# Kernel tuning notes

Hardware: AMD Instinct MI355X
Metric: run time of the kernel (lower is better)

Reference implementation:

```python
import jax, jax.numpy as jnp
import numpy as np

NUM_HEADS = 16
HIDDEN = 1024
HEAD_DIM = HIDDEN // NUM_HEADS
B, L = 1, 2048


def setup_inputs() -> dict:
    key = jax.random.key(0)
    ks = jax.random.split(key, 5)
    scale = 1.0 / np.sqrt(HIDDEN)
    x = jax.random.normal(ks[0], (B, L, HIDDEN), dtype=jnp.float32)
    Wq = jax.random.normal(ks[1], (HIDDEN, HIDDEN), dtype=jnp.float32) * scale
    Wk = jax.random.normal(ks[2], (HIDDEN, HIDDEN), dtype=jnp.float32) * scale
    Wv = jax.random.normal(ks[3], (HIDDEN, HIDDEN), dtype=jnp.float32) * scale
    Wo = jax.random.normal(ks[4], (HIDDEN, HIDDEN), dtype=jnp.float32) * scale
    return {"x": x, "Wq": Wq, "Wk": Wk, "Wv": Wv, "Wo": Wo}


def reference(x, Wq, Wk, Wv, Wo):
    Bx, Lx, _ = x.shape
    # nn.Linear computes x @ W.T (bias=False)
    q = (x @ Wq.T).reshape(Bx, Lx, NUM_HEADS, HEAD_DIM)
    k = (x @ Wk.T).reshape(Bx, Lx, NUM_HEADS, HEAD_DIM)
    v = (x @ Wv.T).reshape(Bx, Lx, NUM_HEADS, HEAD_DIM)
    # elu(.)+1 feature map
    q = jax.nn.elu(q) + 1.0
    k = jax.nn.elu(k) + 1.0
    # causal linear-attention state via cumsum of kv outer products
    kv = jnp.einsum('blhd,blhe->blhde', k, v)           # [B,L,H,D,D]
    kv_cumsum = jnp.cumsum(kv, axis=1)
    k_cumsum = jnp.cumsum(k, axis=1)
    out = jnp.einsum('blhd,blhde->blhe', q, kv_cumsum)   # [B,L,H,D]
    denom = jnp.clip(jnp.einsum('blhd,blhd->blh', q, k_cumsum), 1e-6, None)
    out = out / denom[..., None]
    return out.reshape(Bx, Lx, HIDDEN) @ Wo.T
```

## Files before the change

kernel.cpp:

```cpp
#include <hip/hip_runtime.h>
#include <hip/hip_bf16.h>

typedef __attribute__((ext_vector_type(8))) short short8;
typedef __attribute__((ext_vector_type(4))) float floatx4;
typedef __attribute__((ext_vector_type(8))) unsigned short ushortx8;
typedef __attribute__((ext_vector_type(4))) unsigned short ushortx4;
typedef unsigned short u16;

#define HIDDEN 1024
#define NH 16
#define HD 64
#define SEQ 2048
#define CHUNK 128
#define NCHUNK (SEQ / CHUNK)

__device__ __forceinline__ u16 f2bf(float f) {
    union { float f; unsigned u; } v; v.f = f;
    unsigned r = v.u + 0x7fffu + ((v.u >> 16) & 1u);
    return (u16)(r >> 16);
}
__device__ __forceinline__ float bf2f(u16 u) {
    union { unsigned u; float f; } v; v.u = ((unsigned)u) << 16;
    return v.f;
}

__device__ __forceinline__ void gl_lds16(const u16* g, u16* l) {
    __builtin_amdgcn_global_load_lds(
        (const __attribute__((address_space(1))) void*)g,
        (__attribute__((address_space(3))) void*)l,
        16, 0, 0);
}

__global__ __launch_bounds__(256)
void convert_all(const float* __restrict__ x,  const float* __restrict__ Wq,
                 const float* __restrict__ Wk, const float* __restrict__ Wv,
                 const float* __restrict__ Wo,
                 u16* __restrict__ xb, u16* __restrict__ Wb, u16* __restrict__ Wob)
{
    const int total4 = 1572864;
    for (int idx = blockIdx.x * 256 + threadIdx.x; idx < total4; idx += gridDim.x * 256) {
        const float4* src; u16* dst; int off;
        if (idx < 524288)       { src = (const float4*)x;  dst = xb;            off = idx; }
        else if (idx < 786432)  { src = (const float4*)Wq; dst = Wb;            off = idx - 524288; }
        else if (idx < 1048576) { src = (const float4*)Wk; dst = Wb + 1048576;  off = idx - 786432; }
        else if (idx < 1310720) { src = (const float4*)Wv; dst = Wb + 2097152;  off = idx - 1048576; }
        else                    { src = (const float4*)Wo; dst = Wob;           off = idx - 1310720; }
        float4 v = src[off];
        ushortx4 u = { f2bf(v.x), f2bf(v.y), f2bf(v.z), f2bf(v.w) };
        *(ushortx4*)(dst + (size_t)off * 4) = u;
    }
}

__global__ __launch_bounds__(256, 3)
void qkv_gemm64(const u16* __restrict__ A, const u16* __restrict__ Bm,
                u16* __restrict__ qkb, u16* __restrict__ kT_b, u16* __restrict__ vT_b)
{
    __shared__ u16 As[64 * 64];
    __shared__ u16 Bs[128 * 64];
    const int n0 = blockIdx.x * 128, m0 = blockIdx.y * 64;
    const int t = threadIdx.x;
    const int lane = t & 63, wave = t >> 6;
    const int ln = lane & 15, q4 = lane >> 4;
    const int wm = (wave >> 1) * 32, wn = (wave & 1) * 64;
    const int r_in = t >> 3;
    const int csw = (((t & 7) ^ (r_in & 7)) << 3);

    const u16* Ag = A + (size_t)(m0 + r_in) * 1024 + csw;
    const u16* Bg = Bm + (size_t)(n0 + r_in) * 1024 + csw;

    floatx4 acc[2][4];
#pragma unroll
    for (int i = 0; i < 2; i++)
#pragma unroll
        for (int j = 0; j < 4; j++) acc[i][j] = (floatx4)0.0f;

    for (int k0 = 0; k0 < 1024; k0 += 64) {
        if (k0) __syncthreads();
        gl_lds16(Ag, &As[t * 8]);
        gl_lds16(Ag + 32 * 1024, &As[2048 + t * 8]);
#pragma unroll
        for (int i = 0; i < 4; i++)
            gl_lds16(Bg + (size_t)i * 32 * 1024, &Bs[i * 2048 + t * 8]);
        Ag += 64; Bg += 64;
        __syncthreads();
#pragma unroll
        for (int s = 0; s < 2; s++) {
            const int rc = (((s * 4 + q4) ^ (ln & 7)) << 3);
            short8 af[2], bfr[4];
#pragma unroll
            for (int i = 0; i < 2; i++)
                af[i] = *(const short8*)&As[(wm + i * 16 + ln) * 64 + rc];
#pragma unroll
            for (int j = 0; j < 4; j++)
                bfr[j] = *(const short8*)&Bs[(wn + j * 16 + ln) * 64 + rc];
#pragma unroll
            for (int i = 0; i < 2; i++)
#pragma unroll
                for (int j = 0; j < 4; j++)
                    acc[i][j] = __builtin_amdgcn_mfma_f32_16x16x32_bf16(af[i], bfr[j], acc[i][j], 0, 0, 0);
        }
    }
    const int grp = n0 >> 10;
#pragma unroll
    for (int i = 0; i < 2; i++)
#pragma unroll
        for (int j = 0; j < 4; j++) {
            const int mb = m0 + wm + i * 16 + q4 * 4;
            const int n = n0 + wn + j * 16 + ln;
            const int nh = n & 1023, h = nh >> 6, e = nh & 63;
            float vals[4];
#pragma unroll
            for (int r = 0; r < 4; r++) {
                float v = acc[i][j][r];
                if (grp < 2) v = (v > 0.f) ? (v + 1.f) : __expf(v);
                vals[r] = v;
            }
            if (grp == 0) {
#pragma unroll
                for (int r = 0; r < 4; r++) qkb[(size_t)(mb + r) * 2048 + nh] = f2bf(vals[r]);
            } else if (grp == 1) {
#pragma unroll
                for (int r = 0; r < 4; r++) qkb[(size_t)(mb + r) * 2048 + 1024 + nh] = f2bf(vals[r]);
                ushortx4 u = { f2bf(vals[0]), f2bf(vals[1]), f2bf(vals[2]), f2bf(vals[3]) };
                *(ushortx4*)&kT_b[(size_t)(h * 64 + e) * 2048 + mb] = u;
            } else {
                ushortx4 u = { f2bf(vals[0]), f2bf(vals[1]), f2bf(vals[2]), f2bf(vals[3]) };
                *(ushortx4*)&vT_b[(size_t)(h * 64 + e) * 2048 + mb] = u;
            }
        }
}

__global__ __launch_bounds__(256, 2)
void chunk_stats2(const u16* __restrict__ kT_b, const u16* __restrict__ vT_b,
                  float* __restrict__ S_ws, float* __restrict__ ksum_ws)
{
    __shared__ u16 kT_l[64 * 128];
    __shared__ u16 vT_l[64 * 128];
    const int c = blockIdx.x, h = blockIdx.y;
    const int t = threadIdx.x;
    const int lane = t & 63, w = t >> 6;
    const int ln = lane & 15, q4 = lane >> 4;
#pragma unroll
    for (int i = 0; i < 4; i++) {
        const int d0 = w * 16 + i * 4 + (lane >> 4);
        const int cc = lane & 15;
        const size_t gsrc = (size_t)(h * 64 + d0) * 2048 + c * 128 + ((cc ^ (d0 & 7)) << 3);
        gl_lds16(kT_b + gsrc, &kT_l[(w * 16 + i * 4) * 128 + lane * 8]);
        gl_lds16(vT_b + gsrc, &vT_l[(w * 16 + i * 4) * 128 + lane * 8]);
    }
    __syncthreads();
    floatx4 sacc[4];
#pragma unroll
    for (int j = 0; j < 4; j++) sacc[j] = (floatx4)0.0f;
#pragma unroll
    for (int ks = 0; ks < 4; ks++) {
        const int rc = (((ks * 4 + q4) ^ (ln & 7)) << 3);
        short8 af = *(const short8*)&kT_l[(w * 16 + ln) * 128 + rc];
#pragma unroll
        for (int j = 0; j < 4; j++) {
            short8 bfr = *(const short8*)&vT_l[(j * 16 + ln) * 128 + rc];
            sacc[j] = __builtin_amdgcn_mfma_f32_16x16x32_bf16(af, bfr, sacc[j], 0, 0, 0);
        }
    }
    float* Sp = S_ws + ((size_t)(h * NCHUNK + c) << 12);
#pragma unroll
    for (int j = 0; j < 4; j++)
#pragma unroll
        for (int r = 0; r < 4; r++) {
            int d = w * 16 + q4 * 4 + r;
            int e = j * 16 + ln;
            Sp[e * 64 + d] = sacc[j][r];
        }
    if (t < 64) {
        float s = 0.f;
#pragma unroll
        for (int cc = 0; cc < 16; cc++) {
            ushortx8 v8 = *(const ushortx8*)&kT_l[t * 128 + cc * 8];
#pragma unroll
            for (int jj = 0; jj < 8; jj++) s += bf2f(v8[jj]);
        }
        ksum_ws[(h * NCHUNK + c) * 64 + t] = s;
    }
}

__global__ __launch_bounds__(256, 1)
void attn_out2(const u16* __restrict__ qkb, const u16* __restrict__ vT_b,
               const float* __restrict__ S_ws, const float* __restrict__ ksum_ws,
               u16* __restrict__ attnb)
{
    __shared__ __align__(16) u16 smem[29824];
    u16* q_l   = smem;
    u16* k_l   = smem + 8192;
    u16* kvT_l = smem + 16384;
    u16* P_l   = smem;
    u16* vT_l  = smem + 20992;
    float* kpref  = (float*)(smem + 29184);
    float* denom2 = kpref + 64;

    const int c = blockIdx.x, h = blockIdx.y;
    const int t = threadIdx.x;
    const int lane = t & 63, w = t >> 6;
    const int ln = lane & 15, q4 = lane >> 4;

#pragma unroll
    for (int i = 0; i < 4; i++) {
        const int l = i * 32 + w * 8 + (lane >> 3);
        const int cc = lane & 7;
        const size_t gq = (size_t)(c * CHUNK + l) * 2048 + h * 64 + ((cc ^ (l & 7)) << 3);
        gl_lds16(qkb + gq,        &q_l[(i * 32 + w * 8) * 64 + lane * 8]);
        gl_lds16(qkb + gq + 1024, &k_l[(i * 32 + w * 8) * 64 + lane * 8]);
        const int d0 = w * 16 + i * 4 + (lane >> 4);
        const int cv = lane & 15;
        gl_lds16(vT_b + (size_t)(h * 64 + d0) * 2048 + c * 128 + ((cv ^ (d0 & 7)) << 3),
                 &vT_l[(w * 16 + i * 4) * 128 + lane * 8]);
    }
    {
        const int e = t >> 2, db = (t & 3) * 16;
        float kv[16];
#pragma unroll
        for (int i = 0; i < 16; i++) kv[i] = 0.f;
        for (int cp = 0; cp < c; cp++) {
            const float* Sp = S_ws + ((size_t)(h * NCHUNK + cp) << 12) + e * 64 + db;
#pragma unroll
            for (int g = 0; g < 4; g++) {
                float4 s4 = *(const float4*)(Sp + g * 4);
                kv[g * 4 + 0] += s4.x; kv[g * 4 + 1] += s4.y;
                kv[g * 4 + 2] += s4.z; kv[g * 4 + 3] += s4.w;
            }
        }
#pragma unroll
        for (int g = 0; g < 4; g++) {
            ushortx4 u = { f2bf(kv[g * 4 + 0]), f2bf(kv[g * 4 + 1]),
                           f2bf(kv[g * 4 + 2]), f2bf(kv[g * 4 + 3]) };
            *(ushortx4*)&kvT_l[e * 72 + db + g * 4] = u;
        }
        if (t < 64) {
            float s = 0.f;
            for (int cp = 0; cp < c; cp++) s += ksum_ws[(h * NCHUNK + cp) * 64 + t];
            kpref[t] = s;
        }
    }
    __syncthreads();

    const int pm = (w >> 1) * 64, pn = (w & 1) * 64;
    floatx4 pacc[4][4];
#pragma unroll
    for (int i = 0; i < 4; i++)
#pragma unroll
        for (int j = 0; j < 4; j++) pacc[i][j] = (floatx4)0.0f;
#pragma unroll
    for (int s = 0; s < 2; s++) {
        const int rc = (((s * 4 + q4) ^ (ln & 7)) << 3);
        short8 af[4], bfr[4];
#pragma unroll
        for (int i = 0; i < 4; i++)
            af[i] = *(const short8*)&q_l[(pm + i * 16 + ln) * 64 + rc];
#pragma unroll
        for (int j = 0; j < 4; j++)
            bfr[j] = *(const short8*)&k_l[(pn + j * 16 + ln) * 64 + rc];
#pragma unroll
        for (int i = 0; i < 4; i++)
#pragma unroll
            for (int j = 0; j < 4; j++)
                pacc[i][j] = __builtin_amdgcn_mfma_f32_16x16x32_bf16(af[i], bfr[j], pacc[i][j], 0, 0, 0);
    }
#pragma unroll
    for (int i = 0; i < 4; i++)
#pragma unroll
        for (int r = 0; r < 4; r++) {
            int rowi = pm + i * 16 + q4 * 4 + r;
            float rs = 0.f;
#pragma unroll
            for (int j = 0; j < 4; j++) {
                int col = pn + j * 16 + ln;
                float p = pacc[i][j][r];
                if (col > rowi) p = 0.f;
                pacc[i][j][r] = p;
                rs += p;
            }
#pragma unroll
            for (int off = 1; off < 16; off <<= 1) rs += __shfl_xor(rs, off, 64);
            if (ln == 0) denom2[(w & 1) * 128 + rowi] = rs;
        }
    const int ob = w * 32;
    floatx4 oacc[2][4];
#pragma unroll
    for (int i = 0; i < 2; i++)
#pragma unroll
        for (int j = 0; j < 4; j++) oacc[i][j] = (floatx4)0.0f;
#pragma unroll
    for (int s = 0; s < 2; s++) {
        const int rc = (((s * 4 + q4) ^ (ln & 7)) << 3);
        short8 af[2], bfr[4];
#pragma unroll
        for (int i2 = 0; i2 < 2; i2++)
            af[i2] = *(const short8*)&q_l[(ob + i2 * 16 + ln) * 64 + rc];
#pragma unroll
        for (int j = 0; j < 4; j++)
            bfr[j] = *(const short8*)&kvT_l[(j * 16 + ln) * 72 + s * 32 + q4 * 8];
#pragma unroll
        for (int i2 = 0; i2 < 2; i2++)
#pragma unroll
            for (int j = 0; j < 4; j++)
                oacc[i2][j] = __builtin_amdgcn_mfma_f32_16x16x32_bf16(af[i2], bfr[j], oacc[i2][j], 0, 0, 0);
    }
    __syncthreads();
    if (t < 128) {
        float s = 0.f;
#pragma unroll
        for (int c8 = 0; c8 < 8; c8++) {
            ushortx8 v8 = *(const ushortx8*)&q_l[t * 64 + ((c8 ^ (t & 7)) << 3)];
#pragma unroll
            for (int jj = 0; jj < 8; jj++) s += bf2f(v8[jj]) * kpref[c8 * 8 + jj];
        }
        denom2[t] += s;
    }
    __syncthreads();
#pragma unroll
    for (int i = 0; i < 4; i++)
#pragma unroll
        for (int j = 0; j < 4; j++)
#pragma unroll
            for (int r = 0; r < 4; r++) {
                int rowi = pm + i * 16 + q4 * 4 + r;
                int col = pn + j * 16 + ln;
                P_l[rowi * 136 + col] = f2bf(pacc[i][j][r]);
            }
    __syncthreads();
    for (int ks = 0; ks <= w; ks++) {
        short8 af[2], bfr[4];
#pragma unroll
        for (int i2 = 0; i2 < 2; i2++)
            af[i2] = *(const short8*)&P_l[(ob + i2 * 16 + ln) * 136 + ks * 32 + q4 * 8];
        const int rc = (((ks * 4 + q4) ^ (ln & 7)) << 3);
#pragma unroll
        for (int j = 0; j < 4; j++)
            bfr[j] = *(const short8*)&vT_l[(j * 16 + ln) * 128 + rc];
#pragma unroll
        for (int i2 = 0; i2 < 2; i2++)
#pragma unroll
            for (int j = 0; j < 4; j++)
                oacc[i2][j] = __builtin_amdgcn_mfma_f32_16x16x32_bf16(af[i2], bfr[j], oacc[i2][j], 0, 0, 0);
    }
#pragma unroll
    for (int i2 = 0; i2 < 2; i2++)
#pragma unroll
        for (int j = 0; j < 4; j++)
#pragma unroll
            for (int r = 0; r < 4; r++) {
                int rowi = ob + i2 * 16 + q4 * 4 + r;
                int e = j * 16 + ln;
                float den = denom2[rowi] + denom2[128 + rowi];
                den = fmaxf(den, 1e-6f);
                float val = oacc[i2][j][r] / den;
                attnb[(size_t)(c * CHUNK + rowi) * HIDDEN + h * HD + e] = f2bf(val);
            }
}

__global__ __launch_bounds__(256, 3)
void out_gemm64(const u16* __restrict__ A, const u16* __restrict__ Bm,
                float* __restrict__ out)
{
    __shared__ u16 As[64 * 64];
    __shared__ u16 Bs[64 * 64];
    const int n0 = blockIdx.x * 64, m0 = blockIdx.y * 64;
    const int t = threadIdx.x;
    const int lane = t & 63, wave = t >> 6;
    const int ln = lane & 15, q4 = lane >> 4;
    const int wm = (wave >> 1) * 32, wn = (wave & 1) * 32;
    const int r_in = t >> 3;
    const int csw = (((t & 7) ^ (r_in & 7)) << 3);

    const u16* Ag = A + (size_t)(m0 + r_in) * 1024 + csw;
    const u16* Bg = Bm + (size_t)(n0 + r_in) * 1024 + csw;

    floatx4 acc[2][2];
#pragma unroll
    for (int i = 0; i < 2; i++)
#pragma unroll
        for (int j = 0; j < 2; j++) acc[i][j] = (floatx4)0.0f;

    for (int k0 = 0; k0 < 1024; k0 += 64) {
        if (k0) __syncthreads();
        gl_lds16(Ag, &As[t * 8]);
        gl_lds16(Ag + 32 * 1024, &As[2048 + t * 8]);
        gl_lds16(Bg, &Bs[t * 8]);
        gl_lds16(Bg + 32 * 1024, &Bs[2048 + t * 8]);
        Ag += 64; Bg += 64;
        __syncthreads();
#pragma unroll
        for (int s = 0; s < 2; s++) {
            const int rc = (((s * 4 + q4) ^ (ln & 7)) << 3);
            short8 af[2], bfr[2];
#pragma unroll
            for (int i = 0; i < 2; i++)
                af[i] = *(const short8*)&As[(wm + i * 16 + ln) * 64 + rc];
#pragma unroll
            for (int j = 0; j < 2; j++)
                bfr[j] = *(const short8*)&Bs[(wn + j * 16 + ln) * 64 + rc];
#pragma unroll
            for (int i = 0; i < 2; i++)
#pragma unroll
                for (int j = 0; j < 2; j++)
                    acc[i][j] = __builtin_amdgcn_mfma_f32_16x16x32_bf16(af[i], bfr[j], acc[i][j], 0, 0, 0);
        }
    }
#pragma unroll
    for (int i = 0; i < 2; i++)
#pragma unroll
        for (int j = 0; j < 2; j++)
#pragma unroll
            for (int r = 0; r < 4; r++) {
                int m = m0 + wm + i * 16 + q4 * 4 + r;
                int n = n0 + wn + j * 16 + ln;
                out[(size_t)m * 1024 + n] = acc[i][j][r];
            }
}

extern "C" void kernel_launch(void* const* d_in, const int* in_sizes, int n_in,
                              void* d_out, int out_size, void* d_ws, size_t ws_size,
                              hipStream_t stream)
{
    const float* x  = (const float*)d_in[0];
    const float* Wq = (const float*)d_in[1];
    const float* Wk = (const float*)d_in[2];
    const float* Wv = (const float*)d_in[3];
    const float* Wo = (const float*)d_in[4];
    float* out = (float*)d_out;

    char* ws = (char*)d_ws;
    const size_t MB = 1024 * 1024;
    u16* xb    = (u16*)(ws);
    u16* Wb    = (u16*)(ws + 4 * MB);
    u16* Wob   = (u16*)(ws + 10 * MB);
    u16* qkb   = (u16*)(ws + 12 * MB);
    u16* kT_b  = (u16*)(ws + 20 * MB);
    u16* vT_b  = (u16*)(ws + 24 * MB);
    float* S_ws    = (float*)(ws + 28 * MB);
    float* ksum_ws = (float*)(ws + 32 * MB);
    u16* attnb = (u16*)(ws + 33 * MB);

    convert_all<<<2048, 256, 0, stream>>>(x, Wq, Wk, Wv, Wo, xb, Wb, Wob);
    qkv_gemm64<<<dim3(24, 32), 256, 0, stream>>>(xb, Wb, qkb, kT_b, vT_b);
    chunk_stats2<<<dim3(NCHUNK, NH), 256, 0, stream>>>(kT_b, vT_b, S_ws, ksum_ws);
    attn_out2<<<dim3(NCHUNK, NH), 256, 0, stream>>>(qkb, vT_b, S_ws, ksum_ws, attnb);
    out_gemm64<<<dim3(16, 32), 256, 0, stream>>>(attnb, Wob, out);
}
```

Before: 129.3 us.

## Precompute chunk prefix states in a scan kernel and widen attention blocks

Result: faster. 123.7 us (-4.3%).

```diff
diff --git a/kernel.cpp b/kernel.cpp
--- a/kernel.cpp
+++ b/kernel.cpp
@@ -183,85 +183,92 @@
     }
 }
 
-__global__ __launch_bounds__(256, 1)
+__global__ __launch_bounds__(256)
+void scan_kv(const float* __restrict__ S_ws, const float* __restrict__ ksum_ws,
+             u16* __restrict__ kvpref_b, float* __restrict__ kspref)
+{
+    const int h = blockIdx.x, qt = blockIdx.y;
+    const int t = threadIdx.x;
+    const int li = qt * 1024 + t * 4;
+    const int e = li >> 6, d0 = li & 63;
+    const int slot = e * 64 + ((((d0 >> 3) ^ (e & 7)) << 3) | (d0 & 7));
+    float a0 = 0.f, a1 = 0.f, a2 = 0.f, a3 = 0.f;
+    for (int c = 0; c < 16; c++) {
+        ushortx4 u = { f2bf(a0), f2bf(a1), f2bf(a2), f2bf(a3) };
+        *(ushortx4*)&kvpref_b[(((size_t)(h * 16 + c)) << 12) + slot] = u;
+        float4 s4 = *(const float4*)(S_ws + (((size_t)(h * 16 + c)) << 12) + li);
+        a0 += s4.x; a1 += s4.y; a2 += s4.z; a3 += s4.w;
+    }
+    if (qt == 0 && t < 64) {
+        float a = 0.f;
+        for (int c = 0; c < 16; c++) {
+            kspref[(h * 16 + c) * 64 + t] = a;
+            a += ksum_ws[(h * 16 + c) * 64 + t];
+        }
+    }
+}
+
+__global__ __launch_bounds__(512, 2)
 void attn_out2(const u16* __restrict__ qkb, const u16* __restrict__ vT_b,
-               const float* __restrict__ S_ws, const float* __restrict__ ksum_ws,
+               const u16* __restrict__ kvpref_b, const float* __restrict__ kspref,
                u16* __restrict__ attnb)
 {
     __shared__ __align__(16) u16 smem[29824];
     u16* q_l   = smem;
     u16* k_l   = smem + 8192;
     u16* kvT_l = smem + 16384;
+    u16* vT_l  = smem + 20480;
     u16* P_l   = smem;
-    u16* vT_l  = smem + 20992;
-    float* kpref  = (float*)(smem + 29184);
-    float* denom2 = kpref + 64;
+    float* kpref  = (float*)(smem + 28672);
+    float* denom4 = kpref + 64;
 
     const int c = blockIdx.x, h = blockIdx.y;
     const int t = threadIdx.x;
     const int lane = t & 63, w = t >> 6;
     const int ln = lane & 15, q4 = lane >> 4;
 
-#pragma unroll
-    for (int i = 0; i < 4; i++) {
-        const int l = i * 32 + w * 8 + (lane >> 3);
-        const int cc = lane & 7;
-        const size_t gq = (size_t)(c * CHUNK + l) * 2048 + h * 64 + ((cc ^ (l & 7)) << 3);
-        gl_lds16(qkb + gq,        &q_l[(i * 32 + w * 8) * 64 + lane * 8]);
-        gl_lds16(qkb + gq + 1024, &k_l[(i * 32 + w * 8) * 64 + lane * 8]);
-        const int d0 = w * 16 + i * 4 + (lane >> 4);
-        const int cv = lane & 15;
-        gl_lds16(vT_b + (size_t)(h * 64 + d0) * 2048 + c * 128 + ((cv ^ (d0 & 7)) << 3),
-                 &vT_l[(w * 16 + i * 4) * 128 + lane * 8]);
-    }
     {
-        const int e = t >> 2, db = (t & 3) * 16;
-        float kv[16];
-#pragma unroll
-        for (int i = 0; i < 16; i++) kv[i] = 0.f;
-        for (int cp = 0; cp < c; cp++) {
-            const float* Sp = S_ws + ((size_t)(h * NCHUNK + cp) << 12) + e * 64 + db;
-#pragma unroll
-            for (int g = 0; g < 4; g++) {
-                float4 s4 = *(const float4*)(Sp + g * 4);
-                kv[g * 4 + 0] += s4.x; kv[g * 4 + 1] += s4.y;
-                kv[g * 4 + 2] += s4.z; kv[g * 4 + 3] += s4.w;
-            }
-        }
-#pragma unroll
-        for (int g = 0; g < 4; g++) {
-            ushortx4 u = { f2bf(kv[g * 4 + 0]), f2bf(kv[g * 4 + 1]),
-                           f2bf(kv[g * 4 + 2]), f2bf(kv[g * 4 + 3]) };
-            *(ushortx4*)&kvT_l[e * 72 + db + g * 4] = u;
-        }
-        if (t < 64) {
-            float s = 0.f;
-            for (int cp = 0; cp < c; cp++) s += ksum_ws[(h * NCHUNK + cp) * 64 + t];
-            kpref[t] = s;
-        }
-    }
+        const int row = t >> 3, cc = t & 7;
+        const size_t gq = (size_t)(c * CHUNK + row) * 2048 + h * 64
+                        + (size_t)((cc ^ (row & 7)) << 3);
+        gl_lds16(qkb + gq,        &q_l[t * 8]);
+        gl_lds16(qkb + gq + 1024, &k_l[t * 8]);
+        const int row2 = row + 64;
+        const size_t gq2 = (size_t)(c * CHUNK + row2) * 2048 + h * 64
+                         + (size_t)((cc ^ (row2 & 7)) << 3);
+        gl_lds16(qkb + gq2,        &q_l[4096 + t * 8]);
+        gl_lds16(qkb + gq2 + 1024, &k_l[4096 + t * 8]);
+        const int d = t >> 4, cv = t & 15;
+        gl_lds16(vT_b + (size_t)(h * 64 + d) * 2048 + c * 128 + ((cv ^ (d & 7)) << 3),
+                 &vT_l[t * 8]);
+        const int d2 = d + 32;
+        gl_lds16(vT_b + (size_t)(h * 64 + d2) * 2048 + c * 128 + ((cv ^ (d2 & 7)) << 3),
+                 &vT_l[4096 + t * 8]);
+        gl_lds16(kvpref_b + (((size_t)(h * 16 + c)) << 12) + t * 8, &kvT_l[t * 8]);
+    }
+    if (t < 64) kpref[t] = kspref[(h * 16 + c) * 64 + t];
     __syncthreads();
 
-    const int pm = (w >> 1) * 64, pn = (w & 1) * 64;
-    floatx4 pacc[4][4];
+    const int pm = (w >> 2) * 64, pn = (w & 3) * 32;
+    floatx4 pacc[4][2];
 #pragma unroll
     for (int i = 0; i < 4; i++)
 #pragma unroll
-        for (int j = 0; j < 4; j++) pacc[i][j] = (floatx4)0.0f;
+        for (int j = 0; j < 2; j++) pacc[i][j] = (floatx4)0.0f;
 #pragma unroll
     for (int s = 0; s < 2; s++) {
         const int rc = (((s * 4 + q4) ^ (ln & 7)) << 3);
-        short8 af[4], bfr[4];
+        short8 af[4], bfr[2];
 #pragma unroll
         for (int i = 0; i < 4; i++)
             af[i] = *(const short8*)&q_l[(pm + i * 16 + ln) * 64 + rc];
 #pragma unroll
-        for (int j = 0; j < 4; j++)
+        for (int j = 0; j < 2; j++)
             bfr[j] = *(const short8*)&k_l[(pn + j * 16 + ln) * 64 + rc];
 #pragma unroll
         for (int i = 0; i < 4; i++)
 #pragma unroll
-            for (int j = 0; j < 4; j++)
+            for (int j = 0; j < 2; j++)
                 pacc[i][j] = __builtin_amdgcn_mfma_f32_16x16x32_bf16(af[i], bfr[j], pacc[i][j], 0, 0, 0);
     }
 #pragma unroll
@@ -271,7 +278,7 @@
             int rowi = pm + i * 16 + q4 * 4 + r;
             float rs = 0.f;
 #pragma unroll
-            for (int j = 0; j < 4; j++) {
+            for (int j = 0; j < 2; j++) {
                 int col = pn + j * 16 + ln;
                 float p = pacc[i][j][r];
                 if (col > rowi) p = 0.f;
@@ -280,29 +287,21 @@
             }
 #pragma unroll
             for (int off = 1; off < 16; off <<= 1) rs += __shfl_xor(rs, off, 64);
-            if (ln == 0) denom2[(w & 1) * 128 + rowi] = rs;
-        }
-    const int ob = w * 32;
-    floatx4 oacc[2][4];
-#pragma unroll
-    for (int i = 0; i < 2; i++)
-#pragma unroll
-        for (int j = 0; j < 4; j++) oacc[i][j] = (floatx4)0.0f;
+            if (ln == 0) denom4[(w & 3) * 128 + rowi] = rs;
+        }
+    const int ob = w * 16;
+    floatx4 oacc[4];
+#pragma unroll
+    for (int j = 0; j < 4; j++) oacc[j] = (floatx4)0.0f;
 #pragma unroll
     for (int s = 0; s < 2; s++) {
         const int rc = (((s * 4 + q4) ^ (ln & 7)) << 3);
-        short8 af[2], bfr[4];
-#pragma unroll
-        for (int i2 = 0; i2 < 2; i2++)
-            af[i2] = *(const short8*)&q_l[(ob + i2 * 16 + ln) * 64 + rc];
-#pragma unroll
-        for (int j = 0; j < 4; j++)
-            bfr[j] = *(const short8*)&kvT_l[(j * 16 + ln) * 72 + s * 32 + q4 * 8];
-#pragma unroll
-        for (int i2 = 0; i2 < 2; i2++)
-#pragma unroll
-            for (int j = 0; j < 4; j++)
-                oacc[i2][j] = __builtin_amdgcn_mfma_f32_16x16x32_bf16(af[i2], bfr[j], oacc[i2][j], 0, 0, 0);
+        short8 af = *(const short8*)&q_l[(ob + ln) * 64 + rc];
+#pragma unroll
+        for (int j = 0; j < 4; j++) {
+            short8 bfr = *(const short8*)&kvT_l[(j * 16 + ln) * 64 + rc];
+            oacc[j] = __builtin_amdgcn_mfma_f32_16x16x32_bf16(af, bfr, oacc[j], 0, 0, 0);
+        }
     }
     __syncthreads();
     if (t < 128) {
@@ -313,13 +312,13 @@
 #pragma unroll
             for (int jj = 0; jj < 8; jj++) s += bf2f(v8[jj]) * kpref[c8 * 8 + jj];
         }
-        denom2[t] += s;
+        denom4[t] += s;
     }
     __syncthreads();
 #pragma unroll
     for (int i = 0; i < 4; i++)
 #pragma unroll
-        for (int j = 0; j < 4; j++)
+        for (int j = 0; j < 2; j++)
 #pragma unroll
             for (int r = 0; r < 4; r++) {
                 int rowi = pm + i * 16 + q4 * 4 + r;
@@ -327,34 +326,26 @@
                 P_l[rowi * 136 + col] = f2bf(pacc[i][j][r]);
             }
     __syncthreads();
-    for (int ks = 0; ks <= w; ks++) {
-        short8 af[2], bfr[4];
-#pragma unroll
-        for (int i2 = 0; i2 < 2; i2++)
-            af[i2] = *(const short8*)&P_l[(ob + i2 * 16 + ln) * 136 + ks * 32 + q4 * 8];
+    for (int ks = 0; ks <= (w >> 1); ks++) {
+        short8 af = *(const short8*)&P_l[(ob + ln) * 136 + ks * 32 + q4 * 8];
         const int rc = (((ks * 4 + q4) ^ (ln & 7)) << 3);
 #pragma unroll
-        for (int j = 0; j < 4; j++)
-            bfr[j] = *(const short8*)&vT_l[(j * 16 + ln) * 128 + rc];
-#pragma unroll
-        for (int i2 = 0; i2 < 2; i2++)
-#pragma unroll
-            for (int j = 0; j < 4; j++)
-                oacc[i2][j] = __builtin_amdgcn_mfma_f32_16x16x32_bf16(af[i2], bfr[j], oacc[i2][j], 0, 0, 0);
-    }
-#pragma unroll
-    for (int i2 = 0; i2 < 2; i2++)
-#pragma unroll
-        for (int j = 0; j < 4; j++)
-#pragma unroll
-            for (int r = 0; r < 4; r++) {
-                int rowi = ob + i2 * 16 + q4 * 4 + r;
-                int e = j * 16 + ln;
-                float den = denom2[rowi] + denom2[128 + rowi];
-                den = fmaxf(den, 1e-6f);
-                float val = oacc[i2][j][r] / den;
-                attnb[(size_t)(c * CHUNK + rowi) * HIDDEN + h * HD + e] = f2bf(val);
-            }
+        for (int j = 0; j < 4; j++) {
+            short8 bfr = *(const short8*)&vT_l[(j * 16 + ln) * 128 + rc];
+            oacc[j] = __builtin_amdgcn_mfma_f32_16x16x32_bf16(af, bfr, oacc[j], 0, 0, 0);
+        }
+    }
+#pragma unroll
+    for (int r = 0; r < 4; r++) {
+        const int rowi = ob + q4 * 4 + r;
+        float den = denom4[rowi] + denom4[128 + rowi] + denom4[256 + rowi] + denom4[384 + rowi];
+        den = fmaxf(den, 1e-6f);
+#pragma unroll
+        for (int j = 0; j < 4; j++) {
+            int e = j * 16 + ln;
+            attnb[(size_t)(c * CHUNK + rowi) * HIDDEN + h * HD + e] = f2bf(oacc[j][r] / den);
+        }
+    }
 }
 
 __global__ __launch_bounds__(256, 3)
@@ -439,10 +430,13 @@
     float* S_ws    = (float*)(ws + 28 * MB);
     float* ksum_ws = (float*)(ws + 32 * MB);
     u16* attnb = (u16*)(ws + 33 * MB);
+    u16* kvpref_b = (u16*)(ws + 37 * MB);
+    float* kspref = (float*)(ws + 39 * MB);
 
     convert_all<<<2048, 256, 0, stream>>>(x, Wq, Wk, Wv, Wo, xb, Wb, Wob);
     qkv_gemm64<<<dim3(24, 32), 256, 0, stream>>>(xb, Wb, qkb, kT_b, vT_b);
     chunk_stats2<<<dim3(NCHUNK, NH), 256, 0, stream>>>(kT_b, vT_b, S_ws, ksum_ws);
-    attn_out2<<<dim3(NCHUNK, NH), 256, 0, stream>>>(qkb, vT_b, S_ws, ksum_ws, attnb);
+    scan_kv<<<dim3(NH, 4), 256, 0, stream>>>(S_ws, ksum_ws, kvpref_b, kspref);
+    attn_out2<<<dim3(NCHUNK, NH), 512, 0, stream>>>(qkb, vT_b, kvpref_b, kspref, attnb);
     out_gemm64<<<dim3(16, 32), 256, 0, stream>>>(attnb, Wob, out);
 }
```
